# Kernel optimization log

Hardware: AMD Instinct MI355X
Metric: run time of the kernel (lower is better)

The kernel has to match this reference:

```python
import jax, jax.numpy as jnp
import numpy as np

B, S, H, KV, D, HID = 1, 2048, 32, 8, 128, 4096
SCALE = D ** -0.5
EPS = 1e-5
QMAX = 127.0  # 8-bit symmetric fake quant


def fake_quant(x):
    # per-tensor symmetric int8 fake quantization with straight-through estimator
    s = jnp.maximum(jnp.max(jnp.abs(x)), 1e-5) / QMAX
    q = jnp.clip(jnp.round(x / s), -QMAX - 1.0, QMAX) * s
    return x + jax.lax.stop_gradient(q - x)


def rms_norm(x, w):
    xf = x.astype(jnp.float32)
    var = jnp.mean(xf * xf, axis=-1, keepdims=True)
    return (xf * jax.lax.rsqrt(var + EPS)).astype(x.dtype) * w


def rotate_half(x):
    h = x.shape[-1] // 2
    return jnp.concatenate([-x[..., h:], x[..., :h]], axis=-1)


def qlinear(x, W):
    # QuantLinear: fake-quant activation and weight, then matmul (no bias)
    return fake_quant(x) @ fake_quant(W).T


def setup_inputs() -> dict:
    key = jax.random.key(0)
    ks = jax.random.split(key, 5)
    hidden_states = jax.random.normal(ks[0], (B, S, HID), jnp.float32)
    # RoPE tables
    inv_freq = 1.0 / (10000.0 ** (np.arange(0, D, 2, dtype=np.float32) / D))
    freqs = np.outer(np.arange(S, dtype=np.float32), inv_freq)  # [S, D/2]
    emb = np.concatenate([freqs, freqs], axis=-1)  # [S, D]
    cos = jnp.asarray(np.cos(emb))[None]  # [1,S,D]
    sin = jnp.asarray(np.sin(emb))[None]
    # causal additive mask [1,1,S,S]
    mask = jnp.where(np.tril(np.ones((S, S), dtype=bool)), 0.0, -1e9).astype(jnp.float32)[None, None]
    Wq = jax.random.normal(ks[1], (H * D, HID), jnp.float32) * 0.02
    Wk = jax.random.normal(ks[2], (KV * D, HID), jnp.float32) * 0.02
    Wv = jax.random.normal(ks[3], (KV * D, HID), jnp.float32) * 0.02
    Wo = jax.random.normal(ks[4], (HID, H * D), jnp.float32) * 0.02
    q_norm_w = jnp.ones((D,), jnp.float32)
    k_norm_w = jnp.ones((D,), jnp.float32)
    return dict(hidden_states=hidden_states, cos=cos, sin=sin, attention_mask=mask,
                Wq=Wq, Wk=Wk, Wv=Wv, Wo=Wo, q_norm_w=q_norm_w, k_norm_w=k_norm_w)


def reference(hidden_states, cos, sin, attention_mask, Wq, Wk, Wv, Wo, q_norm_w, k_norm_w):
    b, s, _ = hidden_states.shape
    q = qlinear(hidden_states, Wq).reshape(b, s, H, D).transpose(0, 2, 1, 3)   # [B,H,S,D]
    k = qlinear(hidden_states, Wk).reshape(b, s, KV, D).transpose(0, 2, 1, 3)  # [B,KV,S,D]
    v = qlinear(hidden_states, Wv).reshape(b, s, KV, D).transpose(0, 2, 1, 3)
    q = rms_norm(q, q_norm_w)
    k = rms_norm(k, k_norm_w)
    c = cos[:, None]  # unsqueeze head dim -> [1,1,S,D]
    sn = sin[:, None]
    q = q * c + rotate_half(q) * sn
    k = k * c + rotate_half(k) * sn
    n_rep = H // KV
    k = jnp.repeat(k, n_rep, axis=1)  # [B,H,S,D]
    v = jnp.repeat(v, n_rep, axis=1)
    # fake-quant around QK^T
    q = fake_quant(q)
    k = fake_quant(k)
    scores = jnp.einsum('bhqd,bhkd->bhqk', q, k) * SCALE + attention_mask
    p = jax.nn.softmax(scores.astype(jnp.float32), axis=-1).astype(q.dtype)
    # fake-quant around PV
    p = fake_quant(p)
    v = fake_quant(v)
    out = jnp.einsum('bhqk,bhkd->bhqd', p, v)
    out = out.transpose(0, 2, 1, 3).reshape(b, s, H * D)
    return qlinear(out, Wo)
```

## Files before the change

kernel.cpp:

```cpp
#include <hip/hip_runtime.h>
#include <hip/hip_bf16.h>
#include <math.h>
#include <stdint.h>

#define S_LEN 2048
#define NH    32
#define NKV   8
#define HD    128
#define HIDD  4096

typedef unsigned short u16;
typedef __attribute__((ext_vector_type(4))) int i32x4;

#define GLD16(g, l) __builtin_amdgcn_global_load_lds( \
    (const __attribute__((address_space(1))) void*)(g), \
    (__attribute__((address_space(3))) void*)(l), 16, 0, 0)


__device__ __forceinline__ float slot_scale(const unsigned* slot) {
    return fmaxf(__uint_as_float(*slot), 1e-5f) / 127.0f;
}

__device__ __forceinline__ int qint(float x, float s) {
    float q = rintf(x / s);
    q = fminf(fmaxf(q, -128.0f), 127.0f);
    return (int)q;
}

__device__ __forceinline__ void block_amax_atomic(float m, unsigned* slot) {
    __shared__ float wmax[8];
    const int lane = threadIdx.x & 63;
    const int wid  = threadIdx.x >> 6;
    const int nw   = blockDim.x >> 6;
    #pragma unroll
    for (int o = 32; o; o >>= 1) m = fmaxf(m, __shfl_xor(m, o));
    if (lane == 0) wmax[wid] = m;
    __syncthreads();
    if (threadIdx.x == 0) {
        float bm = wmax[0];
        for (int i = 1; i < nw; ++i) bm = fmaxf(bm, wmax[i]);
        atomicMax(slot, __float_as_uint(bm));
    }
}

struct Amax5Args { const float* p[5]; size_t n4[5]; };
__global__ __launch_bounds__(256) void absmax5_kernel(Amax5Args a, unsigned* slots) {
    const int t = blockIdx.y;
    const float4* x4 = (const float4*)a.p[t];
    const size_t n4 = a.n4[t];
    size_t i = (size_t)blockIdx.x * blockDim.x + threadIdx.x;
    size_t stride = (size_t)gridDim.x * blockDim.x;
    float m = 0.0f;
    for (; i < n4; i += stride) {
        float4 v = x4[i];
        m = fmaxf(m, fmaxf(fmaxf(fabsf(v.x), fabsf(v.y)), fmaxf(fabsf(v.z), fabsf(v.w))));
    }
    block_amax_atomic(m, slots + t);
}

struct Quant5Args { const float* p[5]; char* o[5]; size_t n4[5]; };
__global__ __launch_bounds__(256) void quant5_kernel(Quant5Args a, const unsigned* slots) {
    const int t = blockIdx.y;
    float s = slot_scale(slots + t);
    const float4* x4 = (const float4*)a.p[t];
    unsigned* o4 = (unsigned*)a.o[t];
    const size_t n4 = a.n4[t];
    size_t i = (size_t)blockIdx.x * blockDim.x + threadIdx.x;
    size_t stride = (size_t)gridDim.x * blockDim.x;
    for (; i < n4; i += stride) {
        float4 v = x4[i];
        unsigned o = (unsigned)(qint(v.x, s) & 255)
                   | ((unsigned)(qint(v.y, s) & 255) << 8)
                   | ((unsigned)(qint(v.z, s) & 255) << 16)
                   | ((unsigned)(qint(v.w, s) & 255) << 24);
        o4[i] = o;
    }
}

__global__ __launch_bounds__(256) void quant_kernel(const float* __restrict__ x,
                                                    size_t n4, const unsigned* slot,
                                                    char* __restrict__ out) {
    float s = slot_scale(slot);
    size_t i = (size_t)blockIdx.x * blockDim.x + threadIdx.x;
    size_t stride = (size_t)gridDim.x * blockDim.x;
    const float4* x4 = (const float4*)x;
    unsigned* o4 = (unsigned*)out;
    for (; i < n4; i += stride) {
        float4 v = x4[i];
        unsigned o = (unsigned)(qint(v.x, s) & 255)
                   | ((unsigned)(qint(v.y, s) & 255) << 8)
                   | ((unsigned)(qint(v.z, s) & 255) << 16)
                   | ((unsigned)(qint(v.w, s) & 255) << 24);
        o4[i] = o;
    }
}

__device__ __forceinline__ void gemm_body(const char* __restrict__ A,
                                          const char* __restrict__ B,
                                          float* __restrict__ C,
                                          int m0, int n0, int N, int K,
                                          float scale, unsigned* out_amax,
                                          char* Asm, char* Bsm) {
    const int tid  = threadIdx.x;
    const int lane = tid & 63;
    const int wave = tid >> 6;
    const int wr = (wave >> 1) * 64;
    const int wc = (wave & 1) * 64;
    const int l15 = lane & 15;
    const int l4  = lane >> 4;
    const int cx  = (l4 ^ (l15 & 3)) * 16;
    const int r0  = tid >> 2;
    const int sc  = ((tid & 3) ^ ((tid >> 2) & 3)) * 16;

    i32x4 acc[4][4];
    #pragma unroll
    for (int i = 0; i < 4; ++i)
        #pragma unroll
        for (int j = 0; j < 4; ++j) acc[i][j] = (i32x4){0, 0, 0, 0};

    auto STAGE = [&](int buf, int k0) {
        GLD16(&A[(size_t)(m0 + r0) * K + k0 + sc],      &Asm[buf * 8192 + wave * 1024]);
        GLD16(&A[(size_t)(m0 + 64 + r0) * K + k0 + sc], &Asm[buf * 8192 + 4096 + wave * 1024]);
        GLD16(&B[(size_t)(n0 + r0) * K + k0 + sc],      &Bsm[buf * 8192 + wave * 1024]);
        GLD16(&B[(size_t)(n0 + 64 + r0) * K + k0 + sc], &Bsm[buf * 8192 + 4096 + wave * 1024]);
    };

    STAGE(0, 0);
    __syncthreads();
    int cur = 0;
    const int NT = K >> 6;
    for (int t = 0; t < NT; ++t) {
        if (t + 1 < NT) STAGE(cur ^ 1, (t + 1) << 6);
        i32x4 af[4], bfr[4];
        #pragma unroll
        for (int i = 0; i < 4; ++i)
            af[i] = *(const i32x4*)&Asm[cur * 8192 + (wr + i * 16 + l15) * 64 + cx];
        #pragma unroll
        for (int j = 0; j < 4; ++j)
            bfr[j] = *(const i32x4*)&Bsm[cur * 8192 + (wc + j * 16 + l15) * 64 + cx];
        #pragma unroll
        for (int i = 0; i < 4; ++i)
            #pragma unroll
            for (int j = 0; j < 4; ++j)
                acc[i][j] = __builtin_amdgcn_mfma_i32_16x16x64_i8(af[i], bfr[j], acc[i][j], 0, 0, 0);
        __syncthreads();
        cur ^= 1;
    }

    float lm = 0.0f;
    #pragma unroll
    for (int i = 0; i < 4; ++i)
        #pragma unroll
        for (int j = 0; j < 4; ++j)
            #pragma unroll
            for (int r = 0; r < 4; ++r) {
                int row = m0 + wr + i * 16 + l4 * 4 + r;
                int col = n0 + wc + j * 16 + l15;
                float v = (float)acc[i][j][r] * scale;
                C[(size_t)row * N + col] = v;
                lm = fmaxf(lm, fabsf(v));
            }
    if (out_amax) block_amax_atomic(lm, out_amax);
}

__global__ __launch_bounds__(256) void gemm_qkv_kernel(const char* __restrict__ Aq,
                                                       const char* __restrict__ Wqq,
                                                       const char* __restrict__ Wkq,
                                                       const char* __restrict__ Wvq,
                                                       float* __restrict__ qf,
                                                       float* __restrict__ kf,
                                                       float* __restrict__ vf,
                                                       const unsigned* __restrict__ slots,
                                                       unsigned* v_amax) {
    __shared__ __align__(16) char Asm[2 * 8192];
    __shared__ __align__(16) char Bsm[2 * 8192];
    int bid = blockIdx.x;
    int swz = (bid & 7) * 96 + (bid >> 3);
    int x = swz & 15, y = swz >> 4;
    const char* B; float* C; int N, nb; const unsigned* sB; unsigned* am = nullptr;
    if (y < 32)      { B = Wqq; C = qf; N = NH * HD;  nb = y;      sB = slots + 1; }
    else if (y < 40) { B = Wkq; C = kf; N = NKV * HD; nb = y - 32; sB = slots + 2; }
    else             { B = Wvq; C = vf; N = NKV * HD; nb = y - 40; sB = slots + 3; am = v_amax; }
    float scale = slot_scale(slots + 0) * slot_scale(sB);
    gemm_body(Aq, B, C, x * 128, nb * 128, N, HIDD, scale, am, Asm, Bsm);
}

__global__ __launch_bounds__(256) void gemm_o_kernel(const char* __restrict__ A,
                                                     const char* __restrict__ Woq,
                                                     float* __restrict__ C,
                                                     const unsigned* __restrict__ slots) {
    __shared__ __align__(16) char Asm[2 * 8192];
    __shared__ __align__(16) char Bsm[2 * 8192];
    int bid = blockIdx.x;
    int swz = (bid & 7) * 64 + (bid >> 3);
    int x = swz & 15, y = swz >> 4;
    float scale = slot_scale(slots + 8) * slot_scale(slots + 4);
    gemm_body(A, Woq, C, x * 128, y * 128, NH * HD, HIDD, scale, nullptr, Asm, Bsm);
}

__global__ __launch_bounds__(256) void rmsrope2_kernel(float* __restrict__ qx,
                                                       float* __restrict__ kx,
                                                       const float* __restrict__ cosb,
                                                       const float* __restrict__ sinb,
                                                       const float* __restrict__ qw,
                                                       const float* __restrict__ kw,
                                                       unsigned* slots) {
    const int which = blockIdx.y;
    float* x = which ? kx : qx;
    const float* w = which ? kw : qw;
    const int s_shift = which ? 3 : 5;
    const int nrows = which ? (S_LEN * NKV) : (S_LEN * NH);
    unsigned* slot = slots + (which ? 6 : 5);

    const int lane = threadIdx.x & 63;
    const int wid  = threadIdx.x >> 6;
    const float wa = w[lane];
    const float wb = w[lane + 64];
    float lm = 0.0f;
    for (int row = blockIdx.x * 4 + wid; row < nrows; row += gridDim.x * 4) {
        int s = row >> s_shift;
        float* xr = x + (size_t)row * 128;
        float a = xr[lane], b = xr[lane + 64];
        float ss = a * a + b * b;
        #pragma unroll
        for (int o = 32; o; o >>= 1) ss += __shfl_xor(ss, o);
        float inv = 1.0f / sqrtf(ss * (1.0f / 128.0f) + 1e-5f);
        float ya = (a * inv) * wa;
        float yb = (b * inv) * wb;
        const float* cr = cosb + (size_t)s * 128;
        const float* sr = sinb + (size_t)s * 128;
        float o0 = ya * cr[lane]      - yb * sr[lane];
        float o1 = yb * cr[lane + 64] + ya * sr[lane + 64];
        xr[lane] = o0;
        xr[lane + 64] = o1;
        lm = fmaxf(lm, fmaxf(fabsf(o0), fabsf(o1)));
    }
    block_amax_atomic(lm, slot);
}

__global__ __launch_bounds__(256) void quant_qk2_kernel(const float* __restrict__ qx,
                                                        const float* __restrict__ kx,
                                                        const unsigned* slots,
                                                        char* __restrict__ qq,
                                                        char* __restrict__ kq) {
    int tid = blockIdx.x * 256 + threadIdx.x;
    const int qtot = S_LEN * NH * HD;
    if (tid < qtot) {
        float s = slot_scale(slots + 5);
        int d  = tid & 127;
        int h  = (tid >> 7) & 31;
        int sp = tid >> 12;
        qq[((size_t)h * S_LEN + sp) * 128 + d] = (char)qint(qx[tid], s);
    } else {
        tid -= qtot;
        float s = slot_scale(slots + 6);
        int d  = tid & 127;
        int h  = (tid >> 7) & 7;
        int sp = tid >> 10;
        kq[((size_t)h * S_LEN + sp) * 128 + d] = (char)qint(kx[tid], s);
    }
}

__global__ __launch_bounds__(256) void quant_v_kernel(const float* __restrict__ x,
                                                      const unsigned* slot,
                                                      char* __restrict__ out) {
    __shared__ unsigned char t8[64][36];
    const float s = slot_scale(slot);
    const int t   = threadIdx.x;
    const int sp0 = blockIdx.x * 64;
    const int d0  = blockIdx.y * 32;
    const int kvh = blockIdx.z;
    const int dl = t & 31;
    const int sb = t >> 5;
    #pragma unroll
    for (int j = 0; j < 8; ++j) {
        int spl = sb + j * 8;
        float v = x[((size_t)(sp0 + spl) * NKV + kvh) * 128 + d0 + dl];
        t8[spl][dl] = (unsigned char)qint(v, s);
    }
    __syncthreads();
    const int dd = t >> 3;
    const int ch = t & 7;
    unsigned lo = 0, hi = 0;
    #pragma unroll
    for (int j = 0; j < 4; ++j) lo |= (unsigned)t8[ch * 8 + j][dd] << (8 * j);
    #pragma unroll
    for (int j = 0; j < 4; ++j) hi |= (unsigned)t8[ch * 8 + 4 + j][dd] << (8 * j);
    *(uint2*)&out[((size_t)kvh * 128 + d0 + dd) * S_LEN + sp0 + ch * 8] = make_uint2(lo, hi);
}

__global__ __launch_bounds__(256) void attn_kernel(const char* __restrict__ Qq,
                                                   const char* __restrict__ Kq,
                                                   const char* __restrict__ Vt,
                                                   const unsigned* sq_slot,
                                                   const unsigned* sk_slot,
                                                   const unsigned* sv_slot,
                                                   float* __restrict__ O,
                                                   unsigned* amax_slot) {
    __shared__ __align__(16) char Klds[64 * 144];
    __shared__ __align__(16) char Vlds[128 * 80];
    __shared__ __align__(16) char plds[4][16 * 80];

    const int tid  = threadIdx.x;
    const int lane = tid & 63;
    const int wave = tid >> 6;
    const int h  = blockIdx.y;
    const int kv = h >> 2;
    const int l15 = lane & 15;
    const int l4  = lane >> 4;
    const size_t kvS = (size_t)kv * S_LEN;

    const int qt  = 31 - (int)blockIdx.x;
    const int qr0 = qt * 64 + wave * 16;
    const int kb_last = qt * 4 + wave;
    const int nchunk  = qt + 1;

    const float sq = slot_scale(sq_slot);
    const float sk = slot_scale(sk_slot);
    const float sv = slot_scale(sv_slot);
    const float qk_scale = sq * sk * 0.08838834764831845f;
    const float osc = (1.0f / 127.0f) * sv;
    const float NEG = -1e30f;

    i32x4 qf2[2];
    {
        const char* qp = Qq + ((size_t)h * S_LEN + qr0 + l15) * 128 + l4 * 16;
        qf2[0] = *(const i32x4*)(qp);
        qf2[1] = *(const i32x4*)(qp + 64);
    }

    float m_l = NEG, l_l = 0.0f;
    i32x4 kreg[2];
    #pragma unroll
    for (int c = 0; c < 2; ++c) {
        int idx = c * 256 + tid;
        kreg[c] = *(const i32x4*)&Kq[(kvS + (idx >> 3)) * 128 + (idx & 7) * 16];
    }
    #pragma unroll 1
    for (int kc = 0; kc < nchunk; ++kc) {
        __syncthreads();
        #pragma unroll
        for (int c = 0; c < 2; ++c) {
            int idx = c * 256 + tid;
            *(i32x4*)&Klds[(idx >> 3) * 144 + (idx & 7) * 16] = kreg[c];
        }
        __syncthreads();
        if (kc + 1 < nchunk) {
            #pragma unroll
            for (int c = 0; c < 2; ++c) {
                int idx = c * 256 + tid;
                kreg[c] = *(const i32x4*)&Kq[(kvS + (kc + 1) * 64 + (idx >> 3)) * 128 + (idx & 7) * 16];
            }
        }
        #pragma unroll
        for (int hb = 0; hb < 4; ++hb) {
            int kb = kc * 4 + hb;
            if (kb > kb_last) continue;
            i32x4 sacc = {0, 0, 0, 0};
            #pragma unroll
            for (int c = 0; c < 2; ++c) {
                i32x4 kfa = *(const i32x4*)&Klds[(hb * 16 + l15) * 144 + c * 64 + l4 * 16];
                sacc = __builtin_amdgcn_mfma_i32_16x16x64_i8(kfa, qf2[c], sacc, 0, 0, 0);
            }
            const bool diagb = (kb == kb_last);
            float sc[4];
            float bm = NEG;
            #pragma unroll
            for (int r = 0; r < 4; ++r) {
                float x = (float)sacc[r] * qk_scale;
                bool msk = diagb && ((l4 * 4 + r) > l15);
                sc[r] = x;
                bm = fmaxf(bm, msk ? NEG : x);
            }
            float mn = fmaxf(m_l, bm);
            float corr = __expf(m_l - mn);
            float ps = 0.0f;
            #pragma unroll
            for (int r = 0; r < 4; ++r) {
                bool msk = diagb && ((l4 * 4 + r) > l15);
                float p = msk ? 0.0f : __expf(sc[r] - mn);
                ps += p;
            }
            l_l = l_l * corr + ps;
            m_l = mn;
        }
    }
    float m2 = fmaxf(m_l, __shfl_xor(m_l, 16));
    float mfin = fmaxf(m2, __shfl_xor(m2, 32));
    float t = l_l * __expf(m_l - mfin);
    t += __shfl_xor(t, 16);
    t += __shfl_xor(t, 32);
    float rl = 127.0f / t;

    i32x4 oacc[8];
    #pragma unroll
    for (int dt = 0; dt < 8; ++dt) oacc[dt] = (i32x4){0, 0, 0, 0};

    i32x4 vreg[2];
    #pragma unroll
    for (int c = 0; c < 2; ++c) {
        int idx = c * 256 + tid;
        kreg[c] = *(const i32x4*)&Kq[(kvS + (idx >> 3)) * 128 + (idx & 7) * 16];
        vreg[c] = *(const i32x4*)&Vt[((size_t)kv * 128 + (idx >> 2)) * S_LEN + (idx & 3) * 16];
    }
    #pragma unroll 1
    for (int kc = 0; kc < nchunk; ++kc) {
        __syncthreads();
        #pragma unroll
        for (int c = 0; c < 2; ++c) {
            int idx = c * 256 + tid;
            *(i32x4*)&Klds[(idx >> 3) * 144 + (idx & 7) * 16] = kreg[c];
            *(i32x4*)&Vlds[(idx >> 2) * 80 + (idx & 3) * 16] = vreg[c];
        }
        __syncthreads();
        if (kc + 1 < nchunk) {
            #pragma unroll
            for (int c = 0; c < 2; ++c) {
                int idx = c * 256 + tid;
                kreg[c] = *(const i32x4*)&Kq[(kvS + (kc + 1) * 64 + (idx >> 3)) * 128 + (idx & 7) * 16];
                vreg[c] = *(const i32x4*)&Vt[((size_t)kv * 128 + (idx >> 2)) * S_LEN + (kc + 1) * 64 + (idx & 3) * 16];
            }
        }
        #pragma unroll
        for (int hb = 0; hb < 4; ++hb) {
            int kb = kc * 4 + hb;
            unsigned pack = 0;
            if (kb <= kb_last) {
                i32x4 sacc = {0, 0, 0, 0};
                #pragma unroll
                for (int c = 0; c < 2; ++c) {
                    i32x4 kfa = *(const i32x4*)&Klds[(hb * 16 + l15) * 144 + c * 64 + l4 * 16];
                    sacc = __builtin_amdgcn_mfma_i32_16x16x64_i8(kfa, qf2[c], sacc, 0, 0, 0);
                }
                const bool diagb = (kb == kb_last);
                #pragma unroll
                for (int r = 0; r < 4; ++r) {
                    float x = (float)sacc[r] * qk_scale;
                    float p = __expf(x - mfin) * rl;
                    float pq = (diagb && ((l4 * 4 + r) > l15)) ? 0.0f : rintf(p);
                    pack |= ((unsigned)(int)pq) << (8 * r);
                }
            }
            *(unsigned*)&plds[wave][l15 * 80 + hb * 16 + l4 * 4] = pack;
        }
        i32x4 pf = *(const i32x4*)&plds[wave][l15 * 80 + l4 * 16];
        #pragma unroll
        for (int dt = 0; dt < 8; ++dt) {
            i32x4 vfb = *(const i32x4*)&Vlds[(dt * 16 + l15) * 80 + l4 * 16];
            oacc[dt] = __builtin_amdgcn_mfma_i32_16x16x64_i8(pf, vfb, oacc[dt], 0, 0, 0);
        }
    }

    float lm = 0.0f;
    #pragma unroll
    for (int dt = 0; dt < 8; ++dt)
        #pragma unroll
        for (int r = 0; r < 4; ++r) {
            int qrow = qr0 + l4 * 4 + r;
            float v = (float)oacc[dt][r] * osc;
            O[(size_t)qrow * (NH * 128) + h * 128 + dt * 16 + l15] = v;
            lm = fmaxf(lm, fabsf(v));
        }
    block_amax_atomic(lm, amax_slot);
}

extern "C" void kernel_launch(void* const* d_in, const int* in_sizes, int n_in,
                              void* d_out, int out_size, void* d_ws, size_t ws_size,
                              hipStream_t stream) {
    const float* hs   = (const float*)d_in[0];
    const float* cosb = (const float*)d_in[1];
    const float* sinb = (const float*)d_in[2];
    const float* Wq   = (const float*)d_in[4];
    const float* Wk   = (const float*)d_in[5];
    const float* Wv   = (const float*)d_in[6];
    const float* Wo   = (const float*)d_in[7];
    const float* qnw  = (const float*)d_in[8];
    const float* knw  = (const float*)d_in[9];
    float* out = (float*)d_out;

    char* ws = (char*)d_ws;
    unsigned* slots = (unsigned*)ws;
    size_t off = 256;
    auto take = [&](size_t bytes) { size_t o = off; off += (bytes + 255) & ~(size_t)255; return o; };
    char*  hsq  = (char*)(ws + take((size_t)S_LEN * HIDD));
    char*  Wqq  = (char*)(ws + take((size_t)NH * HD * HIDD));
    char*  Wkq  = (char*)(ws + take((size_t)NKV * HD * HIDD));
    char*  Wvq  = (char*)(ws + take((size_t)NKV * HD * HIDD));
    char*  Woq  = (char*)(ws + take((size_t)HIDD * NH * HD));
    float* qf   = (float*)(ws + take((size_t)S_LEN * NH * HD * 4));
    float* kf   = (float*)(ws + take((size_t)S_LEN * NKV * HD * 4));
    float* vf   = (float*)(ws + take((size_t)S_LEN * NKV * HD * 4));
    char*  qq   = (char*)(ws + take((size_t)NH * S_LEN * HD));
    char*  kq   = (char*)(ws + take((size_t)NKV * S_LEN * HD));
    char*  vtq  = (char*)(ws + take((size_t)NKV * HD * S_LEN));
    float* attnf = qf;
    char*  attnq = hsq;

    hipMemsetAsync(ws, 0, 64, stream);

    const size_t n_hs = (size_t)S_LEN * HIDD;
    const size_t n_wq = (size_t)NH * HD * HIDD;
    const size_t n_wk = (size_t)NKV * HD * HIDD;

    Amax5Args aa;
    aa.p[0] = hs; aa.p[1] = Wq; aa.p[2] = Wk; aa.p[3] = Wv; aa.p[4] = Wo;
    aa.n4[0] = n_hs / 4; aa.n4[1] = n_wq / 4; aa.n4[2] = n_wk / 4;
    aa.n4[3] = n_wk / 4; aa.n4[4] = n_wq / 4;
    absmax5_kernel<<<dim3(512, 5), 256, 0, stream>>>(aa, slots);

    Quant5Args qa;
    qa.p[0] = hs; qa.p[1] = Wq; qa.p[2] = Wk; qa.p[3] = Wv; qa.p[4] = Wo;
    qa.o[0] = hsq; qa.o[1] = Wqq; qa.o[2] = Wkq; qa.o[3] = Wvq; qa.o[4] = Woq;
    qa.n4[0] = n_hs / 4; qa.n4[1] = n_wq / 4; qa.n4[2] = n_wk / 4;
    qa.n4[3] = n_wk / 4; qa.n4[4] = n_wq / 4;
    quant5_kernel<<<dim3(1024, 5), 256, 0, stream>>>(qa, slots);

    gemm_qkv_kernel<<<768, 256, 0, stream>>>(hsq, Wqq, Wkq, Wvq, qf, kf, vf,
                                             slots, slots + 7);

    rmsrope2_kernel<<<dim3(1024, 2), 256, 0, stream>>>(qf, kf, cosb, sinb, qnw, knw, slots);

    quant_qk2_kernel<<<40960, 256, 0, stream>>>(qf, kf, slots, qq, kq);
    quant_v_kernel<<<dim3(32, 4, 8), 256, 0, stream>>>(vf, slots + 7, vtq);

    attn_kernel<<<dim3(32, NH), 256, 0, stream>>>(qq, kq, vtq,
                                                  slots + 5, slots + 6, slots + 7,
                                                  attnf, slots + 8);

    quant_kernel<<<2048, 256, 0, stream>>>(attnf, n_hs / 4, slots + 8, attnq);
    gemm_o_kernel<<<512, 256, 0, stream>>>(attnq, Woq, out, slots);
    (void)in_sizes; (void)n_in; (void)out_size; (void)ws_size;
}
```

Measured before the change: 410.0 us.

## Pair causal query tiles per block and use exp2 with specialized diagonal paths

Each attention block now processes two query tiles, qt and 31-qt, so every block does the same amount of causal work, and the grid is halved to 16x32. The softmax switches to base-2 exponentials through a raw v_exp_f32 with log2(e) folded into the QK scale. Separate interior and diagonal code paths remove per-element mask checks from non-diagonal key blocks. Halving the grid to 512 blocks may leave compute units idle on the MI355X, and each block now runs its work in sequence.

```diff
diff --git a/kernel.cpp b/kernel.cpp
--- a/kernel.cpp
+++ b/kernel.cpp
@@ -19,6 +19,10 @@
 
 __device__ __forceinline__ float slot_scale(const unsigned* slot) {
     return fmaxf(__uint_as_float(*slot), 1e-5f) / 127.0f;
+}
+
+__device__ __forceinline__ float exp2_fast(float x) {
+    float r; asm("v_exp_f32 %0, %1" : "=v"(r) : "v"(x)); return r;
 }
 
 __device__ __forceinline__ int qint(float x, float s) {
@@ -310,157 +314,189 @@
     const int l4  = lane >> 4;
     const size_t kvS = (size_t)kv * S_LEN;
 
-    const int qt  = 31 - (int)blockIdx.x;
-    const int qr0 = qt * 64 + wave * 16;
-    const int kb_last = qt * 4 + wave;
-    const int nchunk  = qt + 1;
-
     const float sq = slot_scale(sq_slot);
     const float sk = slot_scale(sk_slot);
     const float sv = slot_scale(sv_slot);
-    const float qk_scale = sq * sk * 0.08838834764831845f;
+    const float qs2 = sq * sk * 0.08838834764831845f * 1.4426950408889634f;
     const float osc = (1.0f / 127.0f) * sv;
     const float NEG = -1e30f;
 
-    i32x4 qf2[2];
-    {
-        const char* qp = Qq + ((size_t)h * S_LEN + qr0 + l15) * 128 + l4 * 16;
-        qf2[0] = *(const i32x4*)(qp);
-        qf2[1] = *(const i32x4*)(qp + 64);
-    }
-
-    float m_l = NEG, l_l = 0.0f;
-    i32x4 kreg[2];
-    #pragma unroll
-    for (int c = 0; c < 2; ++c) {
-        int idx = c * 256 + tid;
-        kreg[c] = *(const i32x4*)&Kq[(kvS + (idx >> 3)) * 128 + (idx & 7) * 16];
-    }
+    float lm = 0.0f;
+
     #pragma unroll 1
-    for (int kc = 0; kc < nchunk; ++kc) {
-        __syncthreads();
-        #pragma unroll
-        for (int c = 0; c < 2; ++c) {
-            int idx = c * 256 + tid;
-            *(i32x4*)&Klds[(idx >> 3) * 144 + (idx & 7) * 16] = kreg[c];
+    for (int tpass = 0; tpass < 2; ++tpass) {
+        const int qt  = tpass ? (31 - (int)blockIdx.x) : (int)blockIdx.x;
+        const int qr0 = qt * 64 + wave * 16;
+        const int nchunk = qt + 1;
+
+        i32x4 qf2[2];
+        {
+            const char* qp = Qq + ((size_t)h * S_LEN + qr0 + l15) * 128 + l4 * 16;
+            qf2[0] = *(const i32x4*)(qp);
+            qf2[1] = *(const i32x4*)(qp + 64);
         }
-        __syncthreads();
-        if (kc + 1 < nchunk) {
-            #pragma unroll
-            for (int c = 0; c < 2; ++c) {
-                int idx = c * 256 + tid;
-                kreg[c] = *(const i32x4*)&Kq[(kvS + (kc + 1) * 64 + (idx >> 3)) * 128 + (idx & 7) * 16];
-            }
-        }
-        #pragma unroll
-        for (int hb = 0; hb < 4; ++hb) {
-            int kb = kc * 4 + hb;
-            if (kb > kb_last) continue;
+
+        float m_l = NEG, l_l = 0.0f;
+
+        auto qk_block = [&](int hb) -> i32x4 {
             i32x4 sacc = {0, 0, 0, 0};
             #pragma unroll
             for (int c = 0; c < 2; ++c) {
                 i32x4 kfa = *(const i32x4*)&Klds[(hb * 16 + l15) * 144 + c * 64 + l4 * 16];
                 sacc = __builtin_amdgcn_mfma_i32_16x16x64_i8(kfa, qf2[c], sacc, 0, 0, 0);
             }
-            const bool diagb = (kb == kb_last);
-            float sc[4];
-            float bm = NEG;
+            return sacc;
+        };
+        auto p1_interior = [&](int hb) {
+            i32x4 sacc = qk_block(hb);
+            float x0 = (float)sacc[0] * qs2, x1 = (float)sacc[1] * qs2;
+            float x2 = (float)sacc[2] * qs2, x3 = (float)sacc[3] * qs2;
+            float bm = fmaxf(fmaxf(x0, x1), fmaxf(x2, x3));
+            float mn = fmaxf(m_l, bm);
+            float ps = exp2_fast(x0 - mn) + exp2_fast(x1 - mn)
+                     + exp2_fast(x2 - mn) + exp2_fast(x3 - mn);
+            l_l = l_l * exp2_fast(m_l - mn) + ps;
+            m_l = mn;
+        };
+        auto p1_diag = [&](int hb) {
+            i32x4 sacc = qk_block(hb);
+            float x[4];
             #pragma unroll
             for (int r = 0; r < 4; ++r) {
-                float x = (float)sacc[r] * qk_scale;
-                bool msk = diagb && ((l4 * 4 + r) > l15);
-                sc[r] = x;
-                bm = fmaxf(bm, msk ? NEG : x);
-            }
+                float v = (float)sacc[r] * qs2;
+                x[r] = ((l4 * 4 + r) > l15) ? NEG : v;
+            }
+            float bm = fmaxf(fmaxf(x[0], x[1]), fmaxf(x[2], x[3]));
             float mn = fmaxf(m_l, bm);
-            float corr = __expf(m_l - mn);
-            float ps = 0.0f;
-            #pragma unroll
-            for (int r = 0; r < 4; ++r) {
-                bool msk = diagb && ((l4 * 4 + r) > l15);
-                float p = msk ? 0.0f : __expf(sc[r] - mn);
-                ps += p;
-            }
-            l_l = l_l * corr + ps;
+            float ps = exp2_fast(x[0] - mn) + exp2_fast(x[1] - mn)
+                     + exp2_fast(x[2] - mn) + exp2_fast(x[3] - mn);
+            l_l = l_l * exp2_fast(m_l - mn) + ps;
             m_l = mn;
-        }
-    }
-    float m2 = fmaxf(m_l, __shfl_xor(m_l, 16));
-    float mfin = fmaxf(m2, __shfl_xor(m2, 32));
-    float t = l_l * __expf(m_l - mfin);
-    t += __shfl_xor(t, 16);
-    t += __shfl_xor(t, 32);
-    float rl = 127.0f / t;
-
-    i32x4 oacc[8];
-    #pragma unroll
-    for (int dt = 0; dt < 8; ++dt) oacc[dt] = (i32x4){0, 0, 0, 0};
-
-    i32x4 vreg[2];
-    #pragma unroll
-    for (int c = 0; c < 2; ++c) {
-        int idx = c * 256 + tid;
-        kreg[c] = *(const i32x4*)&Kq[(kvS + (idx >> 3)) * 128 + (idx & 7) * 16];
-        vreg[c] = *(const i32x4*)&Vt[((size_t)kv * 128 + (idx >> 2)) * S_LEN + (idx & 3) * 16];
-    }
-    #pragma unroll 1
-    for (int kc = 0; kc < nchunk; ++kc) {
-        __syncthreads();
+        };
+
+        i32x4 kreg[2];
         #pragma unroll
         for (int c = 0; c < 2; ++c) {
             int idx = c * 256 + tid;
-            *(i32x4*)&Klds[(idx >> 3) * 144 + (idx & 7) * 16] = kreg[c];
-            *(i32x4*)&Vlds[(idx >> 2) * 80 + (idx & 3) * 16] = vreg[c];
+            kreg[c] = *(const i32x4*)&Kq[(kvS + (idx >> 3)) * 128 + (idx & 7) * 16];
         }
-        __syncthreads();
-        if (kc + 1 < nchunk) {
+        #pragma unroll 1
+        for (int kc = 0; kc < nchunk; ++kc) {
+            __syncthreads();
             #pragma unroll
             for (int c = 0; c < 2; ++c) {
                 int idx = c * 256 + tid;
-                kreg[c] = *(const i32x4*)&Kq[(kvS + (kc + 1) * 64 + (idx >> 3)) * 128 + (idx & 7) * 16];
-                vreg[c] = *(const i32x4*)&Vt[((size_t)kv * 128 + (idx >> 2)) * S_LEN + (kc + 1) * 64 + (idx & 3) * 16];
-            }
-        }
-        #pragma unroll
-        for (int hb = 0; hb < 4; ++hb) {
-            int kb = kc * 4 + hb;
-            unsigned pack = 0;
-            if (kb <= kb_last) {
-                i32x4 sacc = {0, 0, 0, 0};
+                *(i32x4*)&Klds[(idx >> 3) * 144 + (idx & 7) * 16] = kreg[c];
+            }
+            __syncthreads();
+            if (kc + 1 < nchunk) {
                 #pragma unroll
                 for (int c = 0; c < 2; ++c) {
-                    i32x4 kfa = *(const i32x4*)&Klds[(hb * 16 + l15) * 144 + c * 64 + l4 * 16];
-                    sacc = __builtin_amdgcn_mfma_i32_16x16x64_i8(kfa, qf2[c], sacc, 0, 0, 0);
+                    int idx = c * 256 + tid;
+                    kreg[c] = *(const i32x4*)&Kq[(kvS + (kc + 1) * 64 + (idx >> 3)) * 128 + (idx & 7) * 16];
                 }
-                const bool diagb = (kb == kb_last);
+            }
+            if (kc < qt) {
+                p1_interior(0); p1_interior(1); p1_interior(2); p1_interior(3);
+            } else {
                 #pragma unroll
-                for (int r = 0; r < 4; ++r) {
-                    float x = (float)sacc[r] * qk_scale;
-                    float p = __expf(x - mfin) * rl;
-                    float pq = (diagb && ((l4 * 4 + r) > l15)) ? 0.0f : rintf(p);
-                    pack |= ((unsigned)(int)pq) << (8 * r);
+                for (int hb = 0; hb < 4; ++hb) {
+                    if (hb < wave) p1_interior(hb);
+                    else if (hb == wave) p1_diag(hb);
                 }
             }
-            *(unsigned*)&plds[wave][l15 * 80 + hb * 16 + l4 * 4] = pack;
         }
-        i32x4 pf = *(const i32x4*)&plds[wave][l15 * 80 + l4 * 16];
-        #pragma unroll
-        for (int dt = 0; dt < 8; ++dt) {
-            i32x4 vfb = *(const i32x4*)&Vlds[(dt * 16 + l15) * 80 + l4 * 16];
-            oacc[dt] = __builtin_amdgcn_mfma_i32_16x16x64_i8(pf, vfb, oacc[dt], 0, 0, 0);
+        float m2 = fmaxf(m_l, __shfl_xor(m_l, 16));
+        float mfin = fmaxf(m2, __shfl_xor(m2, 32));
+        float t = l_l * exp2_fast(m_l - mfin);
+        t += __shfl_xor(t, 16);
+        t += __shfl_xor(t, 32);
+        float rl = 127.0f / t;
+
+        i32x4 oacc[8];
+        #pragma unroll
+        for (int dt = 0; dt < 8; ++dt) oacc[dt] = (i32x4){0, 0, 0, 0};
+
+        auto p2_interior = [&](int hb) -> unsigned {
+            i32x4 sacc = qk_block(hb);
+            unsigned pack = 0;
+            #pragma unroll
+            for (int r = 0; r < 4; ++r) {
+                float x = (float)sacc[r] * qs2;
+                float pq = rintf(exp2_fast(x - mfin) * rl);
+                pack |= ((unsigned)(int)pq) << (8 * r);
+            }
+            return pack;
+        };
+        auto p2_diag = [&](int hb) -> unsigned {
+            i32x4 sacc = qk_block(hb);
+            unsigned pack = 0;
+            #pragma unroll
+            for (int r = 0; r < 4; ++r) {
+                float x = (float)sacc[r] * qs2;
+                float p = exp2_fast(x - mfin) * rl;
+                float pq = ((l4 * 4 + r) > l15) ? 0.0f : rintf(p);
+                pack |= ((unsigned)(int)pq) << (8 * r);
+            }
+            return pack;
+        };
+
+        i32x4 vreg[2];
+        #pragma unroll
+        for (int c = 0; c < 2; ++c) {
+            int idx = c * 256 + tid;
+            kreg[c] = *(const i32x4*)&Kq[(kvS + (idx >> 3)) * 128 + (idx & 7) * 16];
+            vreg[c] = *(const i32x4*)&Vt[((size_t)kv * 128 + (idx >> 2)) * S_LEN + (idx & 3) * 16];
         }
-    }
-
-    float lm = 0.0f;
-    #pragma unroll
-    for (int dt = 0; dt < 8; ++dt)
-        #pragma unroll
-        for (int r = 0; r < 4; ++r) {
-            int qrow = qr0 + l4 * 4 + r;
-            float v = (float)oacc[dt][r] * osc;
-            O[(size_t)qrow * (NH * 128) + h * 128 + dt * 16 + l15] = v;
-            lm = fmaxf(lm, fabsf(v));
+        #pragma unroll 1
+        for (int kc = 0; kc < nchunk; ++kc) {
+            __syncthreads();
+            #pragma unroll
+            for (int c = 0; c < 2; ++c) {
+                int idx = c * 256 + tid;
+                *(i32x4*)&Klds[(idx >> 3) * 144 + (idx & 7) * 16] = kreg[c];
+                *(i32x4*)&Vlds[(idx >> 2) * 80 + (idx & 3) * 16] = vreg[c];
+            }
+            __syncthreads();
+            if (kc + 1 < nchunk) {
+                #pragma unroll
+                for (int c = 0; c < 2; ++c) {
+                    int idx = c * 256 + tid;
+                    kreg[c] = *(const i32x4*)&Kq[(kvS + (kc + 1) * 64 + (idx >> 3)) * 128 + (idx & 7) * 16];
+                    vreg[c] = *(const i32x4*)&Vt[((size_t)kv * 128 + (idx >> 2)) * S_LEN + (kc + 1) * 64 + (idx & 3) * 16];
+                }
+            }
+            if (kc < qt) {
+                #pragma unroll
+                for (int hb = 0; hb < 4; ++hb)
+                    *(unsigned*)&plds[wave][l15 * 80 + hb * 16 + l4 * 4] = p2_interior(hb);
+            } else {
+                #pragma unroll
+                for (int hb = 0; hb < 4; ++hb) {
+                    unsigned pack = 0;
+                    if (hb < wave) pack = p2_interior(hb);
+                    else if (hb == wave) pack = p2_diag(hb);
+                    *(unsigned*)&plds[wave][l15 * 80 + hb * 16 + l4 * 4] = pack;
+                }
+            }
+            i32x4 pf = *(const i32x4*)&plds[wave][l15 * 80 + l4 * 16];
+            #pragma unroll
+            for (int dt = 0; dt < 8; ++dt) {
+                i32x4 vfb = *(const i32x4*)&Vlds[(dt * 16 + l15) * 80 + l4 * 16];
+                oacc[dt] = __builtin_amdgcn_mfma_i32_16x16x64_i8(pf, vfb, oacc[dt], 0, 0, 0);
+            }
         }
+
+        #pragma unroll
+        for (int dt = 0; dt < 8; ++dt)
+            #pragma unroll
+            for (int r = 0; r < 4; ++r) {
+                int qrow = qr0 + l4 * 4 + r;
+                float v = (float)oacc[dt][r] * osc;
+                O[(size_t)qrow * (NH * 128) + h * 128 + dt * 16 + l15] = v;
+                lm = fmaxf(lm, fabsf(v));
+            }
+    }
     block_amax_atomic(lm, amax_slot);
 }
 
@@ -523,7 +559,7 @@
     quant_qk2_kernel<<<40960, 256, 0, stream>>>(qf, kf, slots, qq, kq);
     quant_v_kernel<<<dim3(32, 4, 8), 256, 0, stream>>>(vf, slots + 7, vtq);
 
-    attn_kernel<<<dim3(32, NH), 256, 0, stream>>>(qq, kq, vtq,
+    attn_kernel<<<dim3(16, NH), 256, 0, stream>>>(qq, kq, vtq,
                                                   slots + 5, slots + 6, slots + 7,
                                                   attnf, slots + 8);
 
```

Result: faster. 361.2 us (-11.9%).
